# Performance work log

Measured on AMD Instinct MI355X. Metric: run time of the kernel, lower is better.

Reference implementation:

```python
import jax, jax.numpy as jnp
import numpy as np

B, T, H = 2, 2048, 1024
NH = 16
D = H // NH  # head_dim = 64
SCALE = D ** -0.5


def setup_inputs() -> dict:
    key = jax.random.key(0)
    ks = jax.random.split(key, 10)
    s_in = 1.0 / np.sqrt(H)   # torch Linear init scale for fan_in=H
    s_d = 1.0 / np.sqrt(D)
    return {
        "x":  jax.random.normal(ks[0], (B, T, H), jnp.float32),
        # stacked per-head Q/K projections: [NH, H, D] weights, [NH, D] biases
        "Wq": jax.random.uniform(ks[1], (NH, H, D), jnp.float32, -s_in, s_in),
        "bq": jax.random.uniform(ks[2], (NH, D), jnp.float32, -s_in, s_in),
        "Wk": jax.random.uniform(ks[3], (NH, H, D), jnp.float32, -s_in, s_in),
        "bk": jax.random.uniform(ks[4], (NH, D), jnp.float32, -s_in, s_in),
        # shared V projection H->D
        "Wv": jax.random.uniform(ks[5], (H, D), jnp.float32, -s_in, s_in),
        "bv": jax.random.uniform(ks[6], (D,), jnp.float32, -s_in, s_in),
        # out projection D->H
        "Wo": jax.random.uniform(ks[7], (D, H), jnp.float32, -s_d, s_d),
        "bo": jax.random.uniform(ks[8], (H,), jnp.float32, -s_d, s_d),
    }


def reference(x, Wq, bq, Wk, bk, Wv, bv, Wo, bo):
    # shared value projection: [B,T,D]
    v = jnp.einsum('bth,hd->btd', x, Wv) + bv
    # batched per-head Q/K projections: [NH,B,T,D]
    q = jnp.einsum('bth,nhd->nbtd', x, Wq) + bq[:, None, None, :]
    k = jnp.einsum('bth,nhd->nbtd', x, Wk) + bk[:, None, None, :]
    # scaled causal attention scores: [NH,B,T,T]
    scores = jnp.einsum('nbtd,nbsd->nbts', q, k) * SCALE
    causal = jnp.triu(jnp.ones((T, T), bool), k=1)  # True above diagonal
    scores = jnp.where(causal, -jnp.inf, scores)
    weights = jax.nn.softmax(scores, axis=-1)  # dropout is identity in eval
    # shared V attended per head, then mean over heads: [B,T,D]
    mean_head = jnp.einsum('nbts,bsd->btd', weights, v) / NH
    out = jnp.einsum('btd,dh->bth', mean_head, Wo) + bo
    mean_weights = jnp.mean(weights, axis=0)  # [B,T,T]
    return out, mean_weights
```

## Files before the change

### kernel.cpp

```cpp
#include <hip/hip_runtime.h>
#include <hip/hip_bf16.h>

#define B_ 2
#define T_ 2048
#define H_ 1024
#define NH_ 16
#define D_ 64
#define BT_ (B_*T_)
#define SCALE_ 0.125f
#define LOG2E_ 1.4426950408889634f

typedef _Float16 f16x8 __attribute__((ext_vector_type(8)));
typedef float f32x4 __attribute__((ext_vector_type(4)));

#define MFMA(a,b,c) __builtin_amdgcn_mfma_f32_16x16x32_f16((a),(b),(c),0,0,0)
#define EXP2(x) __builtin_amdgcn_exp2f(x)

typedef const __attribute__((address_space(1))) void GV;
typedef __attribute__((address_space(3))) void LV;

__device__ __forceinline__ size_t toff(int r, int c, int C) {
    return (size_t)((r >> 4) * (C >> 5) + (c >> 5)) * 512 + (size_t)(((c & 31) >> 3) * 128 + (r & 15) * 8 + (c & 7));
}
__device__ __forceinline__ f16x8 frag_ld(const _Float16* base, int rt, int kc, int Cc, int l15, int quad) {
    return *(const f16x8*)(base + (size_t)(rt * Cc + kc) * 512 + quad * 128 + l15 * 8);
}

__global__ __launch_bounds__(256) void k_prep(const float* __restrict__ x,
                                              const float* __restrict__ Wq, const float* __restrict__ Wk,
                                              const float* __restrict__ Wv, const float* __restrict__ Wo,
                                              _Float16* __restrict__ xb, _Float16* __restrict__ wqk,
                                              _Float16* __restrict__ wvt, _Float16* __restrict__ wot,
                                              float* __restrict__ mw) {
    int blk = blockIdx.x, tid = threadIdx.x;
    if (blk < 256) {
        const float* xs = x + ((size_t)blk << 14);
        _Float16* dstb = xb + ((size_t)blk << 14);
#pragma unroll
        for (int it = 0; it < 8; it++) {
            int E = it * 2048 + tid * 8;
            int rr = (E >> 3) & 15;
            int h = (E >> 9) * 32 + ((E >> 7) & 3) * 8;
            const float* p = xs + (size_t)rr * 1024 + h;
            float4 f0 = *(const float4*)p;
            float4 f1 = *(const float4*)(p + 4);
            f16x8 o;
            o[0]=(_Float16)f0.x; o[1]=(_Float16)f0.y; o[2]=(_Float16)f0.z; o[3]=(_Float16)f0.w;
            o[4]=(_Float16)f1.x; o[5]=(_Float16)f1.y; o[6]=(_Float16)f1.z; o[7]=(_Float16)f1.w;
            *(f16x8*)(dstb + E) = o;
        }
    } else if (blk < 384) {
        int ct = blk - 256;
        const float* W = (ct < 64) ? Wq : Wk;
        int head = (ct >> 2) & 15;
        int dbase = (ct & 3) * 16;
        _Float16* dstb = wqk + ((size_t)ct << 14);
#pragma unroll
        for (int it = 0; it < 8; it++) {
            int E = it * 2048 + tid * 8;
            int rr = (E >> 3) & 15;
            int h = (E >> 9) * 32 + ((E >> 7) & 3) * 8;
            const float* src = W + (size_t)head * 65536 + (size_t)h * 64 + dbase + rr;
            f16x8 o;
#pragma unroll
            for (int e = 0; e < 8; e++) o[e] = (_Float16)src[(size_t)e * 64];
            *(f16x8*)(dstb + E) = o;
        }
    } else if (blk < 388) {
        int rt = blk - 384;
        _Float16* dstb = wvt + ((size_t)rt << 14);
#pragma unroll
        for (int it = 0; it < 8; it++) {
            int E = it * 2048 + tid * 8;
            int rr = (E >> 3) & 15;
            int h = (E >> 9) * 32 + ((E >> 7) & 3) * 8;
            const float* src = Wv + (size_t)h * 64 + rt * 16 + rr;
            f16x8 o;
#pragma unroll
            for (int e = 0; e < 8; e++) o[e] = (_Float16)src[(size_t)e * 64];
            *(f16x8*)(dstb + E) = o;
        }
    } else if (blk < 392) {
        int bl = blk - 388;
#pragma unroll
        for (int it = 0; it < 8; it++) {
            int G = bl * 16384 + it * 2048 + tid * 8;
            int rt = G >> 10;
            int rem = G & 1023;
            int rr = (rem >> 3) & 15;
            int dd = (rem >> 9) * 32 + ((rem >> 7) & 3) * 8;
            const float* src = Wo + (size_t)dd * 1024 + rt * 16 + rr;
            f16x8 o;
#pragma unroll
            for (int e = 0; e < 8; e++) o[e] = (_Float16)src[(size_t)e * 1024];
            *(f16x8*)(wot + G) = o;
        }
    } else {
        int iz = blk - 392;
        int b = (iz >= 496) ? 1 : 0;
        int i = iz - b * 496;
        int s64 = (int)((sqrtf(8.f * i + 1.f) + 1.f) * 0.5f);
        if (s64 * (s64 - 1) / 2 > i) s64--;
        if ((s64 + 1) * s64 / 2 <= i) s64++;
        int q64 = i - s64 * (s64 - 1) / 2;
        float4 z = {0.f, 0.f, 0.f, 0.f};
#pragma unroll
        for (int it = 0; it < 4; it++) {
            int idx = it * 256 + tid;
            int r = idx >> 4, c4 = idx & 15;
            *(float4*)&mw[(size_t)(b * T_ + q64 * 64 + r) * T_ + s64 * 64 + c4 * 4] = z;
        }
    }
}

__global__ __launch_bounds__(256) void k_gemm(const _Float16* __restrict__ xb, const _Float16* __restrict__ wqk,
                                              const float* __restrict__ bq, const float* __restrict__ bk,
                                              const _Float16* __restrict__ wvt, const float* __restrict__ bv,
                                              _Float16* __restrict__ qh, _Float16* __restrict__ kh,
                                              _Float16* __restrict__ vt) {
    __shared__ __align__(16) unsigned char smem[32768];
    _Float16* As = (_Float16*)smem;
    _Float16* Bs = (_Float16*)(smem + 16384);
    int tid = threadIdx.x, w = tid >> 6, lane = tid & 63, l15 = lane & 15, quad = lane >> 4;
    if (blockIdx.x >= 512) {
        float (*red)[16][64] = (float(*)[16][64])smem;
        int rt = blockIdx.x - 512;
        f32x4 acc[4];
#pragma unroll
        for (int j = 0; j < 4; j++) acc[j] = (f32x4){0.f, 0.f, 0.f, 0.f};
        for (int q = 0; q < 8; q++) {
            int kc = w * 8 + q;
            f16x8 a = frag_ld(xb, rt, kc, 32, l15, quad);
#pragma unroll
            for (int j = 0; j < 4; j++) {
                f16x8 bb = frag_ld(wvt, j, kc, 32, l15, quad);
                acc[j] = MFMA(a, bb, acc[j]);
            }
        }
#pragma unroll
        for (int j = 0; j < 4; j++)
#pragma unroll
            for (int r = 0; r < 4; r++) red[w][quad * 4 + r][j * 16 + l15] = acc[j][r];
        __syncthreads();
        int r = tid >> 4, dg = tid & 15;
        int b = rt >> 7, tt = (rt & 127) * 16 + r;
        _Float16* vtb = vt + (size_t)b * 131072;
#pragma unroll
        for (int e = 0; e < 4; e++) {
            int d = dg * 4 + e;
            float s = red[0][r][d] + red[1][r][d] + red[2][r][d] + red[3][r][d] + bv[d];
            vtb[toff(d, tt, 2048)] = (_Float16)s;
        }
        return;
    }
    int bm = blockIdx.x >> 4, bn = blockIdx.x & 15;
    int rowbase = (w >> 1) * 64, colbase = (w & 1) * 64;
    f32x4 acc[4][4];
#pragma unroll
    for (int i = 0; i < 4; i++)
#pragma unroll
        for (int j = 0; j < 4; j++) acc[i][j] = (f32x4){0.f, 0.f, 0.f, 0.f};

    for (int kk = 0; kk < 16; kk++) {
        __syncthreads();
#pragma unroll
        for (int p = 0; p < 4; p++) {
            int c = w * 4 + p;
            __builtin_amdgcn_global_load_lds((GV*)(xb  + ((size_t)((bm * 8 + (c >> 1)) * 32 + kk * 2 + (c & 1))) * 512 + lane * 8),
                                             (LV*)(As + c * 512 + lane * 8), 16, 0, 0);
            __builtin_amdgcn_global_load_lds((GV*)(wqk + ((size_t)((bn * 8 + (c >> 1)) * 32 + kk * 2 + (c & 1))) * 512 + lane * 8),
                                             (LV*)(Bs + c * 512 + lane * 8), 16, 0, 0);
        }
        __syncthreads();
#pragma unroll
        for (int kc = 0; kc < 2; kc++) {
            f16x8 a[4], bf[4];
#pragma unroll
            for (int i = 0; i < 4; i++) a[i]  = *(const f16x8*)&As[((rowbase >> 4) + i) * 1024 + kc * 512 + quad * 128 + l15 * 8];
#pragma unroll
            for (int j = 0; j < 4; j++) bf[j] = *(const f16x8*)&Bs[((colbase >> 4) + j) * 1024 + kc * 512 + quad * 128 + l15 * 8];
#pragma unroll
            for (int i = 0; i < 4; i++)
#pragma unroll
                for (int j = 0; j < 4; j++) acc[i][j] = MFMA(a[i], bf[j], acc[i][j]);
        }
    }
    __syncthreads();
    int b = (bm * 128) >> 11;
    int t_base = (bm * 128) & 2047;
    int rtbase = (t_base + rowbase) >> 4;
    bool isq = (bn < 8);
    int c2base = isq ? (bn * 128 + colbase) : (bn * 128 + colbase - 1024);
    int n = c2base >> 6;
    _Float16* dst = (isq ? qh : kh) + (size_t)(n * 2 + b) * 131072;
    const float* bias_p = isq ? bq : bk;
    float qs = SCALE_ * LOG2E_;
    int i2 = lane >> 4, rowrb = lane & 15;
#pragma unroll
    for (int j = 0; j < 4; j++) {
        float bias = bias_p[c2base + j * 16 + l15];
        _Float16* stg = ((j & 1) ? Bs : As) + w * 1024;
#pragma unroll
        for (int i = 0; i < 4; i++)
#pragma unroll
            for (int r = 0; r < 4; r++) {
                float v = acc[i][j][r] + bias;
                if (isq) v *= qs;
                stg[(i * 16 + quad * 4 + r) * 16 + l15] = (_Float16)v;
            }
#pragma unroll
        for (int oct = 0; oct < 2; oct++) {
            f16x8 val = *(const f16x8*)&stg[(i2 * 16 + rowrb) * 16 + oct * 8];
            int dd0 = j * 16 + oct * 8;
            *(f16x8*)(dst + (size_t)((rtbase + i2) * 2 + (dd0 >> 5)) * 512 + ((dd0 & 31) >> 3) * 128 + rowrb * 8) = val;
        }
    }
}

__global__ __launch_bounds__(256) void k_pass1(const _Float16* __restrict__ qh, const _Float16* __restrict__ kh,
                                               float* __restrict__ lstat4) {
    int tid = threadIdx.x, w = tid >> 6, lane = tid & 63, l15 = lane & 15, quad = lane >> 4;
    int blk = blockIdx.x;
    int nb = blk & 31;
    int s4 = blk >> 5;
    int n = nb >> 1, b = nb & 1;
    const _Float16* qb = qh + (size_t)(n * 2 + b) * 131072;
    const _Float16* kp = kh + (size_t)(n * 2 + b) * 131072;
    int rt0 = s4 * 4;
    f16x8 aq[4][2];
#pragma unroll
    for (int i = 0; i < 4; i++)
#pragma unroll
        for (int kk = 0; kk < 2; kk++) aq[i][kk] = frag_ld(qb, rt0 + i, kk, 2, l15, quad);
    float l[4][4];
#pragma unroll
    for (int i = 0; i < 4; i++)
#pragma unroll
        for (int r = 0; r < 4; r++) l[i][r] = 0.f;
    int total = 4 * s4 + 4;
    int st_lo = (w * total) >> 2;
    int st_hi = ((w + 1) * total) >> 2;
    for (int st = st_lo; st < st_hi; st++) {
        f16x8 c0 = frag_ld(kp, st, 0, 2, l15, quad);
        f16x8 c1 = frag_ld(kp, st, 1, 2, l15, quad);
#pragma unroll
        for (int i = 0; i < 4; i++) {
            if (st > rt0 + i) continue;
            f32x4 sc = (f32x4){0.f, 0.f, 0.f, 0.f};
            sc = MFMA(aq[i][0], c0, sc);
            sc = MFMA(aq[i][1], c1, sc);
            if (st == rt0 + i) {
#pragma unroll
                for (int r = 0; r < 4; r++)
                    if (l15 <= quad * 4 + r) l[i][r] += EXP2(sc[r]);
            } else {
#pragma unroll
                for (int r = 0; r < 4; r++) l[i][r] += EXP2(sc[r]);
            }
        }
    }
#pragma unroll
    for (int off = 1; off < 16; off <<= 1)
#pragma unroll
        for (int i = 0; i < 4; i++)
#pragma unroll
            for (int r = 0; r < 4; r++) l[i][r] += __shfl_xor(l[i][r], off, 64);
    if (l15 == 0) {
        int base = (n * 2 + b) * 2048 + s4 * 64;
#pragma unroll
        for (int i = 0; i < 4; i++)
#pragma unroll
            for (int r = 0; r < 4; r++)
                lstat4[(size_t)(base + i * 16 + quad * 4 + r) * 4 + w] = l[i][r];
    }
}

__global__ __launch_bounds__(256, 6) void k_pass2(const _Float16* __restrict__ qh, const _Float16* __restrict__ kh,
                                                  const float* __restrict__ lstat4,
                                                  float* __restrict__ mw, _Float16* __restrict__ mwh) {
    __shared__ float sl[16][64];
    __shared__ __align__(16) _Float16 kst[2][4096];
    int blk = blockIdx.x;
    int b = (blk >= 528) ? 1 : 0;
    int i0 = blk - 528 * b;
    int i = (i0 & 7) * 66 + (i0 >> 3);
    int p = (int)((sqrtf(8.f * i + 1.f) - 1.f) * 0.5f);
    while (p * (p + 1) / 2 > i) p--;
    while ((p + 1) * (p + 2) / 2 <= i) p++;
    int s64 = i - p * (p + 1) / 2;
    bool masked = (s64 == p);
    int tid = threadIdx.x, w = tid >> 6, lane = tid & 63, l15 = lane & 15, quad = lane >> 4;
    for (int ii = tid; ii < 1024; ii += 256) {
        int h = ii >> 6, r = ii & 63;
        const float4 pl = *(const float4*)&lstat4[(size_t)((h * 2 + b) * 2048 + p * 64 + r) * 4];
        sl[h][r] = -(__log2f(pl.x + pl.y + pl.z + pl.w) + 4.0f);
    }
    int rw = w * 16;
    int rt0 = p * 4 + w;
    int st0 = s64 * 4;
    f32x4 macc[4];
#pragma unroll
    for (int j = 0; j < 4; j++) macc[j] = (f32x4){0.f, 0.f, 0.f, 0.f};

    {
        const _Float16* kp = kh + (size_t)b * 131072;
#pragma unroll
        for (int inst = 0; inst < 2; inst++) {
            int c = inst * 4 + w;
            int gc = (st0 + (c >> 1)) * 2 + (c & 1);
            __builtin_amdgcn_global_load_lds((GV*)(kp + (size_t)gc * 512 + lane * 8),
                                             (LV*)(kst[0] + c * 512 + lane * 8), 16, 0, 0);
        }
    }
    __syncthreads();

    for (int n = 0; n < NH_; n++) {
        if (n < NH_ - 1) {
            const _Float16* kp = kh + (size_t)((n + 1) * 2 + b) * 131072;
#pragma unroll
            for (int inst = 0; inst < 2; inst++) {
                int c = inst * 4 + w;
                int gc = (st0 + (c >> 1)) * 2 + (c & 1);
                __builtin_amdgcn_global_load_lds((GV*)(kp + (size_t)gc * 512 + lane * 8),
                                                 (LV*)(kst[(n + 1) & 1] + c * 512 + lane * 8), 16, 0, 0);
            }
        }
        const _Float16* qb = qh + (size_t)(n * 2 + b) * 131072;
        f16x8 A0 = frag_ld(qb, rt0, 0, 2, l15, quad);
        f16x8 A1 = frag_ld(qb, rt0, 1, 2, l15, quad);
        f32x4 slv = *(const f32x4*)&sl[n][rw + quad * 4];
        const _Float16* ks = kst[n & 1];
#pragma unroll
        for (int j = 0; j < 4; j++) {
            f16x8 K0 = *(const f16x8*)&ks[(j * 2 + 0) * 512 + quad * 128 + l15 * 8];
            f16x8 K1 = *(const f16x8*)&ks[(j * 2 + 1) * 512 + quad * 128 + l15 * 8];
            f32x4 sc = slv;
            sc = MFMA(A0, K0, sc);
            sc = MFMA(A1, K1, sc);
            if (masked) {
                int sg = s64 * 64 + j * 16 + l15;
#pragma unroll
                for (int r = 0; r < 4; r++) {
                    int tg = p * 64 + rw + quad * 4 + r;
                    macc[j][r] += (sg <= tg) ? EXP2(sc[r]) : 0.f;
                }
            } else {
#pragma unroll
                for (int r = 0; r < 4; r++) macc[j][r] += EXP2(sc[r]);
            }
        }
        __syncthreads();
    }
    float* mwb = mw + (size_t)b * T_ * T_;
#pragma unroll
    for (int j = 0; j < 4; j++)
#pragma unroll
        for (int r = 0; r < 4; r++) {
            int tg = p * 64 + rw + quad * 4 + r;
            int sg = s64 * 64 + j * 16 + l15;
            mwb[(size_t)tg * T_ + sg] = macc[j][r];
        }
    _Float16* mhb = mwh + (size_t)b * 4194304;
    _Float16* ws16 = kst[0] + w * 1024;
    int rowrb = lane & 15, qc = lane >> 4;
#pragma unroll
    for (int cc = 0; cc < 2; cc++) {
#pragma unroll
        for (int j2 = 0; j2 < 2; j2++)
#pragma unroll
            for (int r = 0; r < 4; r++) {
                int clw = j2 * 16 + l15;
                ws16[(clw >> 3) * 128 + (quad * 4 + r) * 8 + (clw & 7)] = (_Float16)macc[cc * 2 + j2][r];
            }
        f16x8 val = *(const f16x8*)&ws16[qc * 128 + rowrb * 8];
        *(f16x8*)(mhb + (size_t)(rt0 * 64 + (s64 * 2 + cc)) * 512 + qc * 128 + rowrb * 8) = val;
    }
}

__global__ __launch_bounds__(256) void k_pass3a(const _Float16* __restrict__ mwh, const _Float16* __restrict__ vt,
                                                _Float16* __restrict__ mhp) {
    __shared__ float red[4][16][64];
    int tid = threadIdx.x, w = tid >> 6, lane = tid & 63, l15 = lane & 15, quad = lane >> 4;
    int blk = blockIdx.x;
    int tile = blk >> 3, q = blk & 7;
    int b = tile >> 7, rtb = tile & 127;
    const _Float16* mb = mwh + (size_t)b * 4194304;
    const _Float16* vb = vt + (size_t)b * 131072;
    int nkc = (rtb * 16 + 47) >> 5;
    int qlo = q * 8;
    int qhi = min(qlo + 8, nkc);
    f32x4 acc[4];
#pragma unroll
    for (int j = 0; j < 4; j++) acc[j] = (f32x4){0.f, 0.f, 0.f, 0.f};
    for (int kc = qlo + w; kc < qhi; kc += 4) {
        f16x8 a = frag_ld(mb, rtb, kc, 64, l15, quad);
#pragma unroll
        for (int j = 0; j < 4; j++) {
            f16x8 bb = frag_ld(vb, j, kc, 64, l15, quad);
            acc[j] = MFMA(a, bb, acc[j]);
        }
    }
#pragma unroll
    for (int j = 0; j < 4; j++)
#pragma unroll
        for (int r = 0; r < 4; r++) red[w][quad * 4 + r][j * 16 + l15] = acc[j][r];
    __syncthreads();
    int r = tid >> 4, dg = tid & 15;
    _Float16* dst = mhp + (size_t)q * 262144;
#pragma unroll
    for (int e = 0; e < 4; e++) {
        int d = dg * 4 + e;
        float s = red[0][r][d] + red[1][r][d] + red[2][r][d] + red[3][r][d];
        dst[toff(tile * 16 + r, d, 64)] = (_Float16)s;
    }
}

__global__ __launch_bounds__(256) void k_pass3b(const _Float16* __restrict__ mhp, const _Float16* __restrict__ wot,
                                                const float* __restrict__ bo, float* __restrict__ out0) {
    int bm = blockIdx.x >> 4, bn = blockIdx.x & 15;
    int tid = threadIdx.x, w = tid >> 6, lane = tid & 63, l15 = lane & 15, quad = lane >> 4;
    int rt = bm * 4 + w;
    f16x8 a0[8], a1[8];
#pragma unroll
    for (int q = 0; q < 8; q++) {
        const _Float16* mb = mhp + (size_t)q * 262144;
        a0[q] = frag_ld(mb, rt, 0, 2, l15, quad);
        a1[q] = frag_ld(mb, rt, 1, 2, l15, quad);
    }
    f32x4 acc[4];
#pragma unroll
    for (int j = 0; j < 4; j++) acc[j] = (f32x4){0.f, 0.f, 0.f, 0.f};
#pragma unroll
    for (int j = 0; j < 4; j++) {
        f16x8 b0 = frag_ld(wot, bn * 4 + j, 0, 2, l15, quad);
        f16x8 b1 = frag_ld(wot, bn * 4 + j, 1, 2, l15, quad);
#pragma unroll
        for (int q = 0; q < 8; q++) {
            acc[j] = MFMA(a0[q], b0, acc[j]);
            acc[j] = MFMA(a1[q], b1, acc[j]);
        }
    }
#pragma unroll
    for (int j = 0; j < 4; j++)
#pragma unroll
        for (int r = 0; r < 4; r++) {
            int row = rt * 16 + quad * 4 + r;
            int col = bn * 64 + j * 16 + l15;
            out0[(size_t)row * 1024 + col] = acc[j][r] + bo[col];
        }
}

extern "C" void kernel_launch(void* const* d_in, const int* in_sizes, int n_in,
                              void* d_out, int out_size, void* d_ws, size_t ws_size,
                              hipStream_t stream) {
    const float* x  = (const float*)d_in[0];
    const float* Wq = (const float*)d_in[1];
    const float* bq = (const float*)d_in[2];
    const float* Wk = (const float*)d_in[3];
    const float* bk = (const float*)d_in[4];
    const float* Wv = (const float*)d_in[5];
    const float* bv = (const float*)d_in[6];
    const float* Wo = (const float*)d_in[7];
    const float* bo = (const float*)d_in[8];
    char* ws = (char*)d_ws;
    _Float16* xb    = (_Float16*)(ws + 0);
    _Float16* wqk   = (_Float16*)(ws + 8388608);
    _Float16* wvt   = (_Float16*)(ws + 12582912);
    _Float16* mwh   = (_Float16*)(ws + 0);
    _Float16* qh    = (_Float16*)(ws + 16777216);
    _Float16* kh    = (_Float16*)(ws + 25165824);
    _Float16* vt    = (_Float16*)(ws + 33554432);
    float*    lstat4= (float*)   (ws + 34078720);
    _Float16* mhp   = (_Float16*)(ws + 35127296);
    _Float16* wot   = (_Float16*)(ws + 39321600);
    float* out0 = (float*)d_out;
    float* mw   = out0 + (size_t)BT_ * H_;

    k_prep   <<<1384, 256, 0, stream>>>(x, Wq, Wk, Wv, Wo, xb, wqk, wvt, wot, mw);
    k_gemm   <<<768,  256, 0, stream>>>(xb, wqk, bq, bk, wvt, bv, qh, kh, vt);
    k_pass1  <<<1024, 256, 0, stream>>>(qh, kh, lstat4);
    k_pass2  <<<1056, 256, 0, stream>>>(qh, kh, lstat4, mw, mwh);
    k_pass3a <<<2048, 256, 0, stream>>>(mwh, vt, mhp);
    k_pass3b <<<1024, 256, 0, stream>>>(mhp, wot, bo, out0);
}
```

Measured before the change: 190.2 us.

## Widen pass2 tiles to 64x128 and fuse weights@V with out-projection

Result: no change. 189.8 us (-0.2%).

```diff
diff --git a/kernel.cpp b/kernel.cpp
--- a/kernel.cpp
+++ b/kernel.cpp
@@ -24,6 +24,10 @@
 }
 __device__ __forceinline__ f16x8 frag_ld(const _Float16* base, int rt, int kc, int Cc, int l15, int quad) {
     return *(const f16x8*)(base + (size_t)(rt * Cc + kc) * 512 + quad * 128 + l15 * 8);
+}
+__device__ __forceinline__ int fbase(int p) {
+    int m = p >> 1;
+    return (p & 1) ? (m + 1) * (m + 1) : m * m + m;
 }
 
 __global__ __launch_bounds__(256) void k_prep(const float* __restrict__ x,
@@ -275,20 +279,20 @@
     }
 }
 
-__global__ __launch_bounds__(256, 6) void k_pass2(const _Float16* __restrict__ qh, const _Float16* __restrict__ kh,
+__global__ __launch_bounds__(256, 4) void k_pass2(const _Float16* __restrict__ qh, const _Float16* __restrict__ kh,
                                                   const float* __restrict__ lstat4,
                                                   float* __restrict__ mw, _Float16* __restrict__ mwh) {
     __shared__ float sl[16][64];
-    __shared__ __align__(16) _Float16 kst[2][4096];
+    __shared__ __align__(16) _Float16 kst[2][8192];
     int blk = blockIdx.x;
-    int b = (blk >= 528) ? 1 : 0;
-    int i0 = blk - 528 * b;
-    int i = (i0 & 7) * 66 + (i0 >> 3);
-    int p = (int)((sqrtf(8.f * i + 1.f) - 1.f) * 0.5f);
-    while (p * (p + 1) / 2 > i) p--;
-    while ((p + 1) * (p + 2) / 2 <= i) p++;
-    int s64 = i - p * (p + 1) / 2;
-    bool masked = (s64 == p);
+    int b = (blk >= 272) ? 1 : 0;
+    int i0 = blk - 272 * b;
+    int i = (i0 & 7) * 34 + (i0 >> 3);
+    int p = 2 * (int)sqrtf((float)i);
+    if (p > 31) p = 31;
+    while (fbase(p) > i) p--;
+    while (p < 31 && fbase(p + 1) <= i) p++;
+    int s128 = i - fbase(p);
     int tid = threadIdx.x, w = tid >> 6, lane = tid & 63, l15 = lane & 15, quad = lane >> 4;
     for (int ii = tid; ii < 1024; ii += 256) {
         int h = ii >> 6, r = ii & 63;
@@ -297,15 +301,15 @@
     }
     int rw = w * 16;
     int rt0 = p * 4 + w;
-    int st0 = s64 * 4;
-    f32x4 macc[4];
-#pragma unroll
-    for (int j = 0; j < 4; j++) macc[j] = (f32x4){0.f, 0.f, 0.f, 0.f};
+    int st0 = s128 * 8;
+    f32x4 macc[8];
+#pragma unroll
+    for (int j = 0; j < 8; j++) macc[j] = (f32x4){0.f, 0.f, 0.f, 0.f};
 
     {
         const _Float16* kp = kh + (size_t)b * 131072;
 #pragma unroll
-        for (int inst = 0; inst < 2; inst++) {
+        for (int inst = 0; inst < 4; inst++) {
             int c = inst * 4 + w;
             int gc = (st0 + (c >> 1)) * 2 + (c & 1);
             __builtin_amdgcn_global_load_lds((GV*)(kp + (size_t)gc * 512 + lane * 8),
@@ -318,7 +322,7 @@
         if (n < NH_ - 1) {
             const _Float16* kp = kh + (size_t)((n + 1) * 2 + b) * 131072;
 #pragma unroll
-            for (int inst = 0; inst < 2; inst++) {
+            for (int inst = 0; inst < 4; inst++) {
                 int c = inst * 4 + w;
                 int gc = (st0 + (c >> 1)) * 2 + (c & 1);
                 __builtin_amdgcn_global_load_lds((GV*)(kp + (size_t)gc * 512 + lane * 8),
@@ -331,14 +335,16 @@
         f32x4 slv = *(const f32x4*)&sl[n][rw + quad * 4];
         const _Float16* ks = kst[n & 1];
 #pragma unroll
-        for (int j = 0; j < 4; j++) {
+        for (int j = 0; j < 8; j++) {
+            int s64j = 2 * s128 + (j >> 2);
+            if (s64j > p) continue;
             f16x8 K0 = *(const f16x8*)&ks[(j * 2 + 0) * 512 + quad * 128 + l15 * 8];
             f16x8 K1 = *(const f16x8*)&ks[(j * 2 + 1) * 512 + quad * 128 + l15 * 8];
             f32x4 sc = slv;
             sc = MFMA(A0, K0, sc);
             sc = MFMA(A1, K1, sc);
-            if (masked) {
-                int sg = s64 * 64 + j * 16 + l15;
+            if (s64j == p) {
+                int sg = s128 * 128 + j * 16 + l15;
 #pragma unroll
                 for (int r = 0; r < 4; r++) {
                     int tg = p * 64 + rw + quad * 4 + r;
@@ -353,18 +359,21 @@
     }
     float* mwb = mw + (size_t)b * T_ * T_;
 #pragma unroll
-    for (int j = 0; j < 4; j++)
+    for (int j = 0; j < 8; j++) {
+        if (2 * s128 + (j >> 2) > p) continue;
 #pragma unroll
         for (int r = 0; r < 4; r++) {
             int tg = p * 64 + rw + quad * 4 + r;
-            int sg = s64 * 64 + j * 16 + l15;
+            int sg = s128 * 128 + j * 16 + l15;
             mwb[(size_t)tg * T_ + sg] = macc[j][r];
         }
+    }
     _Float16* mhb = mwh + (size_t)b * 4194304;
     _Float16* ws16 = kst[0] + w * 1024;
     int rowrb = lane & 15, qc = lane >> 4;
 #pragma unroll
-    for (int cc = 0; cc < 2; cc++) {
+    for (int cc = 0; cc < 4; cc++) {
+        if (2 * s128 + (cc >> 1) > p) continue;
 #pragma unroll
         for (int j2 = 0; j2 < 2; j2++)
 #pragma unroll
@@ -373,26 +382,26 @@
                 ws16[(clw >> 3) * 128 + (quad * 4 + r) * 8 + (clw & 7)] = (_Float16)macc[cc * 2 + j2][r];
             }
         f16x8 val = *(const f16x8*)&ws16[qc * 128 + rowrb * 8];
-        *(f16x8*)(mhb + (size_t)(rt0 * 64 + (s64 * 2 + cc)) * 512 + qc * 128 + rowrb * 8) = val;
-    }
-}
-
-__global__ __launch_bounds__(256) void k_pass3a(const _Float16* __restrict__ mwh, const _Float16* __restrict__ vt,
-                                                _Float16* __restrict__ mhp) {
-    __shared__ float red[4][16][64];
+        *(f16x8*)(mhb + (size_t)(rt0 * 64 + (s128 * 4 + cc)) * 512 + qc * 128 + rowrb * 8) = val;
+    }
+}
+
+__global__ __launch_bounds__(512) void k_pass3(const _Float16* __restrict__ mwh, const _Float16* __restrict__ vt,
+                                               const _Float16* __restrict__ wot, const float* __restrict__ bo,
+                                               float* __restrict__ out0) {
+    __shared__ float red[8][16][64];
+    __shared__ __align__(16) _Float16 mhs[1024];
     int tid = threadIdx.x, w = tid >> 6, lane = tid & 63, l15 = lane & 15, quad = lane >> 4;
     int blk = blockIdx.x;
-    int tile = blk >> 3, q = blk & 7;
-    int b = tile >> 7, rtb = tile & 127;
+    int b = blk & 1;
+    int rtb = 127 - (blk >> 1);
     const _Float16* mb = mwh + (size_t)b * 4194304;
     const _Float16* vb = vt + (size_t)b * 131072;
     int nkc = (rtb * 16 + 47) >> 5;
-    int qlo = q * 8;
-    int qhi = min(qlo + 8, nkc);
     f32x4 acc[4];
 #pragma unroll
     for (int j = 0; j < 4; j++) acc[j] = (f32x4){0.f, 0.f, 0.f, 0.f};
-    for (int kc = qlo + w; kc < qhi; kc += 4) {
+    for (int kc = w; kc < nkc; kc += 8) {
         f16x8 a = frag_ld(mb, rtb, kc, 64, l15, quad);
 #pragma unroll
         for (int j = 0; j < 4; j++) {
@@ -405,48 +414,33 @@
 #pragma unroll
         for (int r = 0; r < 4; r++) red[w][quad * 4 + r][j * 16 + l15] = acc[j][r];
     __syncthreads();
-    int r = tid >> 4, dg = tid & 15;
-    _Float16* dst = mhp + (size_t)q * 262144;
-#pragma unroll
-    for (int e = 0; e < 4; e++) {
-        int d = dg * 4 + e;
-        float s = red[0][r][d] + red[1][r][d] + red[2][r][d] + red[3][r][d];
-        dst[toff(tile * 16 + r, d, 64)] = (_Float16)s;
-    }
-}
-
-__global__ __launch_bounds__(256) void k_pass3b(const _Float16* __restrict__ mhp, const _Float16* __restrict__ wot,
-                                                const float* __restrict__ bo, float* __restrict__ out0) {
-    int bm = blockIdx.x >> 4, bn = blockIdx.x & 15;
-    int tid = threadIdx.x, w = tid >> 6, lane = tid & 63, l15 = lane & 15, quad = lane >> 4;
-    int rt = bm * 4 + w;
-    f16x8 a0[8], a1[8];
-#pragma unroll
-    for (int q = 0; q < 8; q++) {
-        const _Float16* mb = mhp + (size_t)q * 262144;
-        a0[q] = frag_ld(mb, rt, 0, 2, l15, quad);
-        a1[q] = frag_ld(mb, rt, 1, 2, l15, quad);
-    }
-    f32x4 acc[4];
-#pragma unroll
-    for (int j = 0; j < 4; j++) acc[j] = (f32x4){0.f, 0.f, 0.f, 0.f};
-#pragma unroll
-    for (int j = 0; j < 4; j++) {
-        f16x8 b0 = frag_ld(wot, bn * 4 + j, 0, 2, l15, quad);
-        f16x8 b1 = frag_ld(wot, bn * 4 + j, 1, 2, l15, quad);
-#pragma unroll
-        for (int q = 0; q < 8; q++) {
-            acc[j] = MFMA(a0[q], b0, acc[j]);
-            acc[j] = MFMA(a1[q], b1, acc[j]);
-        }
-    }
-#pragma unroll
-    for (int j = 0; j < 4; j++)
+    for (int ii = tid; ii < 1024; ii += 512) {
+        int r = ii >> 6, d = ii & 63;
+        float s = red[0][r][d] + red[1][r][d] + red[2][r][d] + red[3][r][d]
+                + red[4][r][d] + red[5][r][d] + red[6][r][d] + red[7][r][d];
+        mhs[(d >> 5) * 512 + ((d & 31) >> 3) * 128 + r * 8 + (d & 7)] = (_Float16)s;
+    }
+    __syncthreads();
+    f16x8 A0 = frag_ld(mhs, 0, 0, 2, l15, quad);
+    f16x8 A1 = frag_ld(mhs, 0, 1, 2, l15, quad);
+    f32x4 acc2[8];
+#pragma unroll
+    for (int j = 0; j < 8; j++) {
+        int ct = w * 8 + j;
+        f16x8 b0 = frag_ld(wot, ct, 0, 2, l15, quad);
+        f16x8 b1 = frag_ld(wot, ct, 1, 2, l15, quad);
+        f32x4 z = (f32x4){0.f, 0.f, 0.f, 0.f};
+        z = MFMA(A0, b0, z);
+        z = MFMA(A1, b1, z);
+        acc2[j] = z;
+    }
+    int rowb = (b * 128 + rtb) * 16 + quad * 4;
+#pragma unroll
+    for (int j = 0; j < 8; j++)
 #pragma unroll
         for (int r = 0; r < 4; r++) {
-            int row = rt * 16 + quad * 4 + r;
-            int col = bn * 64 + j * 16 + l15;
-            out0[(size_t)row * 1024 + col] = acc[j][r] + bo[col];
+            int col = w * 128 + j * 16 + l15;
+            out0[(size_t)(rowb + r) * 1024 + col] = acc2[j][r] + bo[col];
         }
 }
 
@@ -471,7 +465,6 @@
     _Float16* kh    = (_Float16*)(ws + 25165824);
     _Float16* vt    = (_Float16*)(ws + 33554432);
     float*    lstat4= (float*)   (ws + 34078720);
-    _Float16* mhp   = (_Float16*)(ws + 35127296);
     _Float16* wot   = (_Float16*)(ws + 39321600);
     float* out0 = (float*)d_out;
     float* mw   = out0 + (size_t)BT_ * H_;
@@ -479,7 +472,6 @@
     k_prep   <<<1384, 256, 0, stream>>>(x, Wq, Wk, Wv, Wo, xb, wqk, wvt, wot, mw);
     k_gemm   <<<768,  256, 0, stream>>>(xb, wqk, bq, bk, wvt, bv, qh, kh, vt);
     k_pass1  <<<1024, 256, 0, stream>>>(qh, kh, lstat4);
-    k_pass2  <<<1056, 256, 0, stream>>>(qh, kh, lstat4, mw, mwh);
-    k_pass3a <<<2048, 256, 0, stream>>>(mwh, vt, mhp);
-    k_pass3b <<<1024, 256, 0, stream>>>(mhp, wot, bo, out0);
-}
+    k_pass2  <<<544,  256, 0, stream>>>(qh, kh, lstat4, mw, mwh);
+    k_pass3  <<<256,  512, 0, stream>>>(mwh, vt, wot, bo, out0);
+}
```
